# Kernel optimization log

Hardware: AMD Instinct MI355X
Metric: run time of the kernel (lower is better)

Reference implementation:

```python
import jax, jax.numpy as jnp
import numpy as np


def conv1d_same(x, w, b, dilation=1):
    # x: [B, T, Cin], w: [K, Cin, Cout] (WIO), 'same' padding, stride 1
    y = jax.lax.conv_general_dilated(
        x, w, window_strides=(1,), padding='SAME',
        rhs_dilation=(dilation,), dimension_numbers=('NWC', 'WIO', 'NWC'))
    return y + b


def setup_inputs() -> dict:
    key = jax.random.key(0)
    ks = jax.random.split(key, 6)
    B, T, N_IN, N_OUT, ATTN_DIM, KSZ = 16, 2048, 96, 128, 64, 3
    return {
        'x': jax.random.normal(ks[0], (B, T, N_IN), jnp.float32),
        'qkv_w': jax.random.normal(ks[1], (N_IN, 3 * ATTN_DIM), jnp.float32) * 0.05,
        'qkv_b': jnp.zeros((3 * ATTN_DIM,), jnp.float32),
        'scale': jnp.ones((), jnp.float32),
        'conv_w1': jax.random.normal(ks[2], (KSZ, ATTN_DIM, N_OUT), jnp.float32) * 0.05,
        'conv_b1': jnp.zeros((N_OUT,), jnp.float32),
        'conv_w2': jax.random.normal(ks[3], (KSZ, N_OUT, N_OUT), jnp.float32) * 0.05,
        'conv_b2': jnp.zeros((N_OUT,), jnp.float32),
        'down_w': jax.random.normal(ks[4], (N_IN, N_OUT), jnp.float32) * 0.1,
    }


def reference(x, qkv_w, qkv_b, scale, conv_w1, conv_b1, conv_w2, conv_b2, down_w):
    # Dense4Attention: single Dense(3*attn_dim), split into q,k,v
    qkv = x @ qkv_w + qkv_b                       # [B,T,3*D]
    q, k, v = jnp.split(qkv, 3, axis=-1)          # each [B,T,D]
    # AttentionBlock: scores = q k^T * learned scale; non-causal (default)
    scores = jnp.einsum('btd,bsd->bts', q, k) * scale   # [B,T,T]
    weights = jax.nn.softmax(scores, axis=2)            # softmax_axis=2
    out_attn = jnp.einsum('bts,bsd->btd', weights, v)   # [B,T,D]
    h = jax.nn.relu(conv1d_same(out_attn, conv_w1, conv_b1, 1))
    out = jax.nn.relu(conv1d_same(h, conv_w2, conv_b2, 1))   # [B,T,n_out]
    # enhanced residual: softmax over time of row-sums of attn weights
    weight_x = jax.nn.softmax(jnp.sum(weights, axis=2), axis=1)  # [B,T]
    en_res_x = (weight_x[..., None] * x) @ down_w   # n_in != n_out -> downsample
    res = x @ down_w                                 # skip path downsample
    return jax.nn.relu(out + res + en_res_x)
```

## Files before the change

kernel.cpp:

```cpp
#include <hip/hip_runtime.h>
#include <cstdint>

#define B_   16
#define T_   2048
#define CIN  96
#define DH   64
#define NOUT 128

typedef float floatx4 __attribute__((ext_vector_type(4)));
typedef short shortx8 __attribute__((ext_vector_type(8)));
typedef unsigned int uintx2 __attribute__((ext_vector_type(2)));

__device__ __forceinline__ unsigned short f2bf(float f) {
  unsigned int u = __float_as_uint(f);
  u += 0x7FFFu + ((u >> 16) & 1u);
  return (unsigned short)(u >> 16);
}
__device__ __forceinline__ uint32_t cvtpk(float lo, float hi) {
  uint32_t r;
  asm("v_cvt_pk_bf16_f32 %0, %1, %2" : "=v"(r) : "v"(lo), "v"(hi));
  return r;
}
__device__ __forceinline__ floatx4 f4zero() { floatx4 v; v[0]=0.f;v[1]=0.f;v[2]=0.f;v[3]=0.f; return v; }
__device__ __forceinline__ shortx8 s8zero() { shortx8 v;
#pragma unroll
  for (int i=0;i<8;++i) v[i]=0; return v; }

__device__ __forceinline__ void plane_swap(uint32_t& a, uint32_t& b) {
#if __has_builtin(__builtin_amdgcn_permlane32_swap) && __has_builtin(__builtin_amdgcn_permlane16_swap)
  uintx2 r1 = __builtin_amdgcn_permlane32_swap(a, b, false, false);
  uintx2 r2 = __builtin_amdgcn_permlane16_swap(r1[0], r1[1], false, false);
  a = r2[0]; b = r2[1];
#else
  asm volatile("v_permlane32_swap_b32 %0, %1\n\t"
               "v_permlane16_swap_b32 %0, %1"
               : "+v"(a), "+v"(b));
#endif
}

__global__ __launch_bounds__(256) void k_wprep(
    const float* __restrict__ qkv_w, const float* __restrict__ cw1,
    const float* __restrict__ cw2, const float* __restrict__ dw,
    unsigned short* __restrict__ qwt, unsigned short* __restrict__ w1t,
    unsigned short* __restrict__ w2t, unsigned short* __restrict__ dwt)
{
  int o = blockIdx.x * 256 + threadIdx.x;
  if (o < 18432) {
    int co = o / 96, ci = o % 96;
    qwt[o] = f2bf(qkv_w[ci * 192 + co]);
  } else if (o < 43008) {
    int p = o - 18432;
    int tap = p / 8192, rem = p % 8192, co = rem >> 6, ci = rem & 63;
    w1t[p] = f2bf(cw1[(tap * 64 + ci) * 128 + co]);
  } else if (o < 92160) {
    int p = o - 43008;
    int tap = p / 16384, rem = p % 16384, co = rem >> 7, ci = rem & 127;
    w2t[p] = f2bf(cw2[(tap * 128 + ci) * 128 + co]);
  } else if (o < 104448) {
    int p = o - 92160;
    int co = p / 96, ci = p % 96;
    dwt[p] = f2bf(dw[ci * 128 + co]);
  }
}

__global__ __launch_bounds__(256) void k_qkv(
    const float* __restrict__ x, const unsigned short* __restrict__ qwt,
    const float* __restrict__ qkv_b, const float* __restrict__ scale_p,
    unsigned short* __restrict__ qb, unsigned short* __restrict__ kb,
    unsigned short* __restrict__ vT)
{
  __shared__ __align__(16) unsigned short Xs[64][104];
  __shared__ __align__(16) unsigned short Vs[64][72];
  const int bx = blockIdx.x;
  const int b = bx >> 5, t0 = (bx & 31) * 64;
  const int tid = threadIdx.x, wave = tid >> 6, lane = tid & 63;
  const int l15 = lane & 15, quad = lane >> 4;
  const float scl2 = scale_p[0] * 1.4426950408889634f;

  for (int idx = tid; idx < 64 * 24; idx += 256) {
    int r = idx / 24, c = (idx % 24) * 4;
    float4 xv = *(const float4*)(x + ((size_t)(b * T_ + t0 + r)) * CIN + c);
    ushort4 o; o.x = f2bf(xv.x); o.y = f2bf(xv.y); o.z = f2bf(xv.z); o.w = f2bf(xv.w);
    *(ushort4*)(&Xs[r][c]) = o;
  }
  __syncthreads();

  floatx4 acc[4][3];
#pragma unroll
  for (int mt = 0; mt < 4; ++mt)
#pragma unroll
    for (int nt = 0; nt < 3; ++nt) acc[mt][nt] = f4zero();

#pragma unroll
  for (int ks = 0; ks < 3; ++ks) {
    shortx8 wf[3];
#pragma unroll
    for (int nt = 0; nt < 3; ++nt) {
      int j = wave * 48 + nt * 16 + l15;
      wf[nt] = *(const shortx8*)(qwt + (size_t)j * 96 + ks * 32 + quad * 8);
    }
#pragma unroll
    for (int mt = 0; mt < 4; ++mt) {
      shortx8 af = *(const shortx8*)(&Xs[mt * 16 + l15][ks * 32 + quad * 8]);
#pragma unroll
      for (int nt = 0; nt < 3; ++nt)
        acc[mt][nt] = __builtin_amdgcn_mfma_f32_16x16x32_bf16(af, wf[nt], acc[mt][nt], 0, 0, 0);
    }
  }

#pragma unroll
  for (int nt = 0; nt < 3; ++nt) {
    int j0 = wave * 48 + nt * 16;
    int j = j0 + l15;
    float bias = qkv_b[j];
#pragma unroll
    for (int mt = 0; mt < 4; ++mt) {
#pragma unroll
      for (int r = 0; r < 4; ++r) {
        int t = t0 + mt * 16 + quad * 4 + r;
        float v = acc[mt][nt][r] + bias;
        if (j0 < 64)        qb[((size_t)b * T_ + t) * DH + j] = f2bf(v * scl2);
        else if (j0 < 128)  kb[((size_t)b * T_ + t) * DH + (j - 64)] = f2bf(v);
        else                Vs[j - 128][mt * 16 + quad * 4 + r] = f2bf(v);
      }
    }
  }
  __syncthreads();
  for (int idx = tid; idx < 64 * 8; idx += 256) {
    int d = idx >> 3, seg = (idx & 7) * 8;
    *(shortx8*)(vT + ((size_t)b * DH + d) * T_ + t0 + seg) =
        *(const shortx8*)(&Vs[d][seg]);
  }
}

__global__ __launch_bounds__(256) void k_attn(
    const unsigned short* __restrict__ qb, const unsigned short* __restrict__ kb,
    const unsigned short* __restrict__ vT,
    unsigned short* __restrict__ ab)
{
  __shared__ __align__(16) unsigned short Kt[64][72];
  __shared__ __align__(16) unsigned short Vt[80][72];
  const int bx = blockIdx.x;
  const int qt = bx & 31, b = bx >> 5;
  const int tid = threadIdx.x, wave = tid >> 6, lane = tid & 63;
  const int l15 = lane & 15, quad = lane >> 4;

  const unsigned short* qrow = qb + ((size_t)b * T_ + qt * 64 + wave * 16 + l15) * DH;
  shortx8 qf0 = *(const shortx8*)(qrow + quad * 8);
  shortx8 qf1 = *(const shortx8*)(qrow + 32 + quad * 8);

  floatx4 O[5];
#pragma unroll
  for (int i = 0; i < 5; ++i) O[i] = f4zero();

  const unsigned short* kbase = kb + (size_t)b * T_ * DH;
  const unsigned short* vbase = vT + (size_t)b * DH * T_;

  for (int idx = tid; idx < 16 * 72; idx += 256) {
    int r = idx / 72, c = idx % 72;
    Vt[64 + r][c] = (r == 0) ? (unsigned short)0x3F80 : (unsigned short)0;
  }

  const int kr0 = tid >> 3, kc = (tid & 7) * 8;
  shortx8 pk[2], pv[2];
#pragma unroll
  for (int i = 0; i < 2; ++i) {
    pk[i] = *(const shortx8*)(kbase + (size_t)(kr0 + i * 32) * DH + kc);
    pv[i] = *(const shortx8*)(vbase + (size_t)(kr0 + i * 32) * T_ + kc);
  }

  for (int t = 0; t < 32; ++t) {
#pragma unroll
    for (int i = 0; i < 2; ++i) {
      *(shortx8*)(&Kt[kr0 + i * 32][kc]) = pk[i];
      *(shortx8*)(&Vt[kr0 + i * 32][kc]) = pv[i];
    }
    __syncthreads();

    if (t < 31) {
      int s0 = (t + 1) * 64;
#pragma unroll
      for (int i = 0; i < 2; ++i) {
        pk[i] = *(const shortx8*)(kbase + (size_t)(s0 + kr0 + i * 32) * DH + kc);
        pv[i] = *(const shortx8*)(vbase + (size_t)(kr0 + i * 32) * T_ + s0 + kc);
      }
    }

    floatx4 S[4];
#pragma unroll
    for (int nt = 0; nt < 4; ++nt) {
      shortx8 bk0 = *(const shortx8*)(&Kt[nt * 16 + l15][quad * 8]);
      shortx8 bk1 = *(const shortx8*)(&Kt[nt * 16 + l15][32 + quad * 8]);
      S[nt] = f4zero();
      S[nt] = __builtin_amdgcn_mfma_f32_16x16x32_bf16(bk0, qf0, S[nt], 0, 0, 0);
      S[nt] = __builtin_amdgcn_mfma_f32_16x16x32_bf16(bk1, qf1, S[nt], 0, 0, 0);
    }

    uint32_t pkv[8];
#pragma unroll
    for (int nt = 0; nt < 4; ++nt) {
#pragma unroll
      for (int j = 0; j < 2; ++j)
        pkv[nt * 2 + j] = cvtpk(exp2f(S[nt][2 * j]), exp2f(S[nt][2 * j + 1]));
    }

#pragma unroll
    for (int kk = 0; kk < 2; ++kk) {
      uint32_t a0 = pkv[4 * kk + 0], b0 = pkv[4 * kk + 2];
      plane_swap(a0, b0);
      uint32_t a1 = pkv[4 * kk + 1], b1 = pkv[4 * kk + 3];
      plane_swap(a1, b1);
      union { shortx8 s; uint32_t u[4]; } fu;
      fu.u[0] = a0; fu.u[1] = a1; fu.u[2] = b0; fu.u[3] = b1;
#pragma unroll
      for (int dt = 0; dt < 5; ++dt) {
        shortx8 bv = *(const shortx8*)(&Vt[dt * 16 + l15][kk * 32 + quad * 8]);
        O[dt] = __builtin_amdgcn_mfma_f32_16x16x32_bf16(fu.s, bv, O[dt], 0, 0, 0);
      }
    }
    __syncthreads();
  }

  unsigned short* abase = ab + ((size_t)b * T_ + qt * 64 + wave * 16) * DH;
#pragma unroll
  for (int r = 0; r < 4; ++r) {
    float s = __shfl(O[4][r], quad << 4);
    float inv = 1.f / s;
    int row = quad * 4 + r;
#pragma unroll
    for (int dt = 0; dt < 4; ++dt)
      abase[(size_t)row * DH + dt * 16 + l15] = f2bf(O[dt][r] * inv);
  }
}

__global__ __launch_bounds__(256) void k_conv12(
    const unsigned short* __restrict__ ab, const float* __restrict__ x,
    const unsigned short* __restrict__ w1t, const unsigned short* __restrict__ w2t,
    const unsigned short* __restrict__ dwt,
    const float* __restrict__ b1, const float* __restrict__ b2,
    float* __restrict__ out)
{
  __shared__ __align__(16) unsigned short At[82][72];
  __shared__ __align__(16) unsigned short Ht[80][136];
  __shared__ __align__(16) unsigned short Xt[64][104];
  const int bx = blockIdx.x;
  const int b = bx >> 5, t0 = (bx & 31) * 64;
  const int tid = threadIdx.x, wave = tid >> 6, lane = tid & 63;
  const int l15 = lane & 15, quad = lane >> 4;

  for (int idx = tid; idx < 82 * 8; idx += 256) {
    int r = idx >> 3, c = (idx & 7) * 8;
    int t = t0 + r - 9;
    shortx8 v = s8zero();
    if (t >= 0 && t < T_) v = *(const shortx8*)(ab + ((size_t)b * T_ + t) * DH + c);
    *(shortx8*)(&At[r][c]) = v;
  }
  for (int idx = tid; idx < 64 * 24; idx += 256) {
    int r = idx / 24, c = (idx % 24) * 4;
    float4 xv = *(const float4*)(x + ((size_t)(b * T_ + t0 + r)) * CIN + c);
    ushort4 o; o.x = f2bf(xv.x); o.y = f2bf(xv.y); o.z = f2bf(xv.z); o.w = f2bf(xv.w);
    *(ushort4*)(&Xt[r][c]) = o;
  }
  __syncthreads();

  {
    floatx4 acc[5][2];
#pragma unroll
    for (int mt = 0; mt < 5; ++mt) { acc[mt][0] = f4zero(); acc[mt][1] = f4zero(); }

#pragma unroll
    for (int tap = 0; tap < 3; ++tap) {
#pragma unroll
      for (int ks = 0; ks < 2; ++ks) {
        shortx8 wf[2];
#pragma unroll
        for (int ct = 0; ct < 2; ++ct) {
          int co = wave * 32 + ct * 16 + l15;
          wf[ct] = *(const shortx8*)(w1t + ((size_t)tap * 128 + co) * 64 + ks * 32 + quad * 8);
        }
#pragma unroll
        for (int mt = 0; mt < 5; ++mt) {
          shortx8 af = *(const shortx8*)(&At[mt * 16 + l15 + tap][ks * 32 + quad * 8]);
          acc[mt][0] = __builtin_amdgcn_mfma_f32_16x16x32_bf16(af, wf[0], acc[mt][0], 0, 0, 0);
          acc[mt][1] = __builtin_amdgcn_mfma_f32_16x16x32_bf16(af, wf[1], acc[mt][1], 0, 0, 0);
        }
      }
    }

#pragma unroll
    for (int ct = 0; ct < 2; ++ct) {
      int co = wave * 32 + ct * 16 + l15;
      float bias = b1[co];
#pragma unroll
      for (int mt = 0; mt < 5; ++mt)
#pragma unroll
        for (int r = 0; r < 4; ++r) {
          int hr = mt * 16 + quad * 4 + r;
          int t = t0 - 8 + hr;
          unsigned short hv = 0;
          if (t >= 0 && t < T_) hv = f2bf(fmaxf(acc[mt][ct][r] + bias, 0.f));
          Ht[hr][co] = hv;
        }
    }
  }
  __syncthreads();

  floatx4 a2[4][2], ar[4][2];
#pragma unroll
  for (int mt = 0; mt < 4; ++mt) { a2[mt][0]=f4zero(); a2[mt][1]=f4zero(); ar[mt][0]=f4zero(); ar[mt][1]=f4zero(); }

#pragma unroll
  for (int tap = 0; tap < 3; ++tap) {
#pragma unroll
    for (int ks = 0; ks < 4; ++ks) {
      shortx8 wf[2];
#pragma unroll
      for (int ct = 0; ct < 2; ++ct) {
        int co = wave * 32 + ct * 16 + l15;
        wf[ct] = *(const shortx8*)(w2t + ((size_t)tap * 128 + co) * 128 + ks * 32 + quad * 8);
      }
#pragma unroll
      for (int mt = 0; mt < 4; ++mt) {
        shortx8 af = *(const shortx8*)(&Ht[mt * 16 + l15 + 7 + tap][ks * 32 + quad * 8]);
        a2[mt][0] = __builtin_amdgcn_mfma_f32_16x16x32_bf16(af, wf[0], a2[mt][0], 0, 0, 0);
        a2[mt][1] = __builtin_amdgcn_mfma_f32_16x16x32_bf16(af, wf[1], a2[mt][1], 0, 0, 0);
      }
    }
  }
#pragma unroll
  for (int ks = 0; ks < 3; ++ks) {
    shortx8 wf[2];
#pragma unroll
    for (int ct = 0; ct < 2; ++ct) {
      int co = wave * 32 + ct * 16 + l15;
      wf[ct] = *(const shortx8*)(dwt + (size_t)co * 96 + ks * 32 + quad * 8);
    }
#pragma unroll
    for (int mt = 0; mt < 4; ++mt) {
      shortx8 af = *(const shortx8*)(&Xt[mt * 16 + l15][ks * 32 + quad * 8]);
      ar[mt][0] = __builtin_amdgcn_mfma_f32_16x16x32_bf16(af, wf[0], ar[mt][0], 0, 0, 0);
      ar[mt][1] = __builtin_amdgcn_mfma_f32_16x16x32_bf16(af, wf[1], ar[mt][1], 0, 0, 0);
    }
  }

  const float kres = 1.0f + 1.0f / 2048.0f;
#pragma unroll
  for (int ct = 0; ct < 2; ++ct) {
    int co = wave * 32 + ct * 16 + l15;
    float bias = b2[co];
#pragma unroll
    for (int mt = 0; mt < 4; ++mt)
#pragma unroll
      for (int r = 0; r < 4; ++r) {
        int t = t0 + mt * 16 + quad * 4 + r;
        float o2 = fmaxf(a2[mt][ct][r] + bias, 0.f);
        out[((size_t)b * T_ + t) * NOUT + co] = fmaxf(o2 + ar[mt][ct][r] * kres, 0.f);
      }
  }
}

extern "C" void kernel_launch(void* const* d_in, const int* in_sizes, int n_in,
                              void* d_out, int out_size, void* d_ws, size_t ws_size,
                              hipStream_t stream) {
  const float* x      = (const float*)d_in[0];
  const float* qkv_w  = (const float*)d_in[1];
  const float* qkv_b  = (const float*)d_in[2];
  const float* scale  = (const float*)d_in[3];
  const float* cw1    = (const float*)d_in[4];
  const float* cb1    = (const float*)d_in[5];
  const float* cw2    = (const float*)d_in[6];
  const float* cb2    = (const float*)d_in[7];
  const float* dw     = (const float*)d_in[8];

  char* ws = (char*)d_ws;
  unsigned short* qb  = (unsigned short*)(ws + 0);
  unsigned short* kb  = (unsigned short*)(ws + 4194304);
  unsigned short* vT  = (unsigned short*)(ws + 8388608);
  unsigned short* ab  = (unsigned short*)(ws + 12582912);
  unsigned short* qwt = (unsigned short*)(ws + 25165824);
  unsigned short* w1t = (unsigned short*)(ws + 25202688);
  unsigned short* w2t = (unsigned short*)(ws + 25251840);
  unsigned short* dwt = (unsigned short*)(ws + 25350144);

  k_wprep <<<408, 256, 0, stream>>>(qkv_w, cw1, cw2, dw, qwt, w1t, w2t, dwt);
  k_qkv   <<<512, 256, 0, stream>>>(x, qwt, qkv_b, scale, qb, kb, vT);
  k_attn  <<<512, 256, 0, stream>>>(qb, kb, vT, ab);
  k_conv12<<<512, 256, 0, stream>>>(ab, x, w1t, w2t, dwt, cb1, cb2, (float*)d_out);
}
```

Before: 143.2 us.

## Split attention keys across waves with register-direct loads and LDS reduction

The attention kernel now has each wave handle all 64 queries of the block over a disjoint quarter of the key range, loading K and V fragments straight from global memory into registers. This removes the shared-memory K/V staging and the per-tile block barriers. Partial outputs and row sums are combined at the end through a shared-memory reduction. The row sum is now accumulated with VALU adds instead of an extra ones-column MFMA. In exchange the kernel holds more accumulator registers, uses more LDS for the reduction buffers, and does uncoalesced global loads that now go through cache rather than LDS.

```diff
diff --git a/kernel.cpp b/kernel.cpp
--- a/kernel.cpp
+++ b/kernel.cpp
@@ -138,98 +138,114 @@
     const unsigned short* __restrict__ vT,
     unsigned short* __restrict__ ab)
 {
-  __shared__ __align__(16) unsigned short Kt[64][72];
-  __shared__ __align__(16) unsigned short Vt[80][72];
+  __shared__ __align__(16) float OL[4][64][68];
+  __shared__ float SL[4][64];
   const int bx = blockIdx.x;
   const int qt = bx & 31, b = bx >> 5;
   const int tid = threadIdx.x, wave = tid >> 6, lane = tid & 63;
   const int l15 = lane & 15, quad = lane >> 4;
 
-  const unsigned short* qrow = qb + ((size_t)b * T_ + qt * 64 + wave * 16 + l15) * DH;
-  shortx8 qf0 = *(const shortx8*)(qrow + quad * 8);
-  shortx8 qf1 = *(const shortx8*)(qrow + 32 + quad * 8);
-
-  floatx4 O[5];
-#pragma unroll
-  for (int i = 0; i < 5; ++i) O[i] = f4zero();
+  shortx8 qf[4][2];
+#pragma unroll
+  for (int qg = 0; qg < 4; ++qg) {
+    const unsigned short* qrow = qb + ((size_t)b * T_ + qt * 64 + qg * 16 + l15) * DH;
+    qf[qg][0] = *(const shortx8*)(qrow + quad * 8);
+    qf[qg][1] = *(const shortx8*)(qrow + 32 + quad * 8);
+  }
+
+  floatx4 O[4][4];
+#pragma unroll
+  for (int qg = 0; qg < 4; ++qg)
+#pragma unroll
+    for (int dt = 0; dt < 4; ++dt) O[qg][dt] = f4zero();
+  float lsum[4] = {0.f, 0.f, 0.f, 0.f};
 
   const unsigned short* kbase = kb + (size_t)b * T_ * DH;
   const unsigned short* vbase = vT + (size_t)b * DH * T_;
 
-  for (int idx = tid; idx < 16 * 72; idx += 256) {
-    int r = idx / 72, c = idx % 72;
-    Vt[64 + r][c] = (r == 0) ? (unsigned short)0x3F80 : (unsigned short)0;
-  }
-
-  const int kr0 = tid >> 3, kc = (tid & 7) * 8;
-  shortx8 pk[2], pv[2];
-#pragma unroll
-  for (int i = 0; i < 2; ++i) {
-    pk[i] = *(const shortx8*)(kbase + (size_t)(kr0 + i * 32) * DH + kc);
-    pv[i] = *(const shortx8*)(vbase + (size_t)(kr0 + i * 32) * T_ + kc);
-  }
-
-  for (int t = 0; t < 32; ++t) {
-#pragma unroll
-    for (int i = 0; i < 2; ++i) {
-      *(shortx8*)(&Kt[kr0 + i * 32][kc]) = pk[i];
-      *(shortx8*)(&Vt[kr0 + i * 32][kc]) = pv[i];
-    }
-    __syncthreads();
-
-    if (t < 31) {
-      int s0 = (t + 1) * 64;
-#pragma unroll
-      for (int i = 0; i < 2; ++i) {
-        pk[i] = *(const shortx8*)(kbase + (size_t)(s0 + kr0 + i * 32) * DH + kc);
-        pv[i] = *(const shortx8*)(vbase + (size_t)(kr0 + i * 32) * T_ + s0 + kc);
-      }
-    }
-
-    floatx4 S[4];
+  for (int ti = 0; ti < 8; ++ti) {
+    const int s0 = (ti * 4 + wave) * 64;
+    shortx8 bk[4][2], bv[2][4];
 #pragma unroll
     for (int nt = 0; nt < 4; ++nt) {
-      shortx8 bk0 = *(const shortx8*)(&Kt[nt * 16 + l15][quad * 8]);
-      shortx8 bk1 = *(const shortx8*)(&Kt[nt * 16 + l15][32 + quad * 8]);
-      S[nt] = f4zero();
-      S[nt] = __builtin_amdgcn_mfma_f32_16x16x32_bf16(bk0, qf0, S[nt], 0, 0, 0);
-      S[nt] = __builtin_amdgcn_mfma_f32_16x16x32_bf16(bk1, qf1, S[nt], 0, 0, 0);
-    }
-
-    uint32_t pkv[8];
-#pragma unroll
-    for (int nt = 0; nt < 4; ++nt) {
-#pragma unroll
-      for (int j = 0; j < 2; ++j)
-        pkv[nt * 2 + j] = cvtpk(exp2f(S[nt][2 * j]), exp2f(S[nt][2 * j + 1]));
-    }
-
-#pragma unroll
-    for (int kk = 0; kk < 2; ++kk) {
-      uint32_t a0 = pkv[4 * kk + 0], b0 = pkv[4 * kk + 2];
-      plane_swap(a0, b0);
-      uint32_t a1 = pkv[4 * kk + 1], b1 = pkv[4 * kk + 3];
-      plane_swap(a1, b1);
-      union { shortx8 s; uint32_t u[4]; } fu;
-      fu.u[0] = a0; fu.u[1] = a1; fu.u[2] = b0; fu.u[3] = b1;
-#pragma unroll
-      for (int dt = 0; dt < 5; ++dt) {
-        shortx8 bv = *(const shortx8*)(&Vt[dt * 16 + l15][kk * 32 + quad * 8]);
-        O[dt] = __builtin_amdgcn_mfma_f32_16x16x32_bf16(fu.s, bv, O[dt], 0, 0, 0);
-      }
-    }
-    __syncthreads();
-  }
-
-  unsigned short* abase = ab + ((size_t)b * T_ + qt * 64 + wave * 16) * DH;
-#pragma unroll
-  for (int r = 0; r < 4; ++r) {
-    float s = __shfl(O[4][r], quad << 4);
-    float inv = 1.f / s;
-    int row = quad * 4 + r;
+      const unsigned short* kr = kbase + (size_t)(s0 + nt * 16 + l15) * DH;
+      bk[nt][0] = *(const shortx8*)(kr + quad * 8);
+      bk[nt][1] = *(const shortx8*)(kr + 32 + quad * 8);
+    }
+#pragma unroll
+    for (int kk = 0; kk < 2; ++kk)
+#pragma unroll
+      for (int dt = 0; dt < 4; ++dt)
+        bv[kk][dt] = *(const shortx8*)(vbase + (size_t)(dt * 16 + l15) * T_ + s0 + kk * 32 + quad * 8);
+
+#pragma unroll
+    for (int qg = 0; qg < 4; ++qg) {
+      floatx4 S[4];
+#pragma unroll
+      for (int nt = 0; nt < 4; ++nt) {
+        S[nt] = f4zero();
+        S[nt] = __builtin_amdgcn_mfma_f32_16x16x32_bf16(bk[nt][0], qf[qg][0], S[nt], 0, 0, 0);
+        S[nt] = __builtin_amdgcn_mfma_f32_16x16x32_bf16(bk[nt][1], qf[qg][1], S[nt], 0, 0, 0);
+      }
+      uint32_t pkv[8];
+#pragma unroll
+      for (int nt = 0; nt < 4; ++nt)
+#pragma unroll
+        for (int j = 0; j < 2; ++j) {
+          float lo = exp2f(S[nt][2 * j]);
+          float hi = exp2f(S[nt][2 * j + 1]);
+          lsum[qg] += lo + hi;
+          pkv[nt * 2 + j] = cvtpk(lo, hi);
+        }
+#pragma unroll
+      for (int kk = 0; kk < 2; ++kk) {
+        uint32_t a0 = pkv[4 * kk + 0], b0 = pkv[4 * kk + 2];
+        plane_swap(a0, b0);
+        uint32_t a1 = pkv[4 * kk + 1], b1 = pkv[4 * kk + 3];
+        plane_swap(a1, b1);
+        union { shortx8 s; uint32_t u[4]; } fu;
+        fu.u[0] = a0; fu.u[1] = a1; fu.u[2] = b0; fu.u[3] = b1;
+#pragma unroll
+        for (int dt = 0; dt < 4; ++dt)
+          O[qg][dt] = __builtin_amdgcn_mfma_f32_16x16x32_bf16(fu.s, bv[kk][dt], O[qg][dt], 0, 0, 0);
+      }
+    }
+  }
+
+#pragma unroll
+  for (int qg = 0; qg < 4; ++qg) {
+    float v = lsum[qg];
+    v += __shfl_xor(v, 16);
+    v += __shfl_xor(v, 32);
+    if (lane < 16) SL[wave][qg * 16 + lane] = v;
 #pragma unroll
     for (int dt = 0; dt < 4; ++dt)
-      abase[(size_t)row * DH + dt * 16 + l15] = f2bf(O[dt][r] * inv);
+#pragma unroll
+      for (int r = 0; r < 4; ++r)
+        OL[wave][qg * 16 + quad * 4 + r][dt * 16 + l15] = O[qg][dt][r];
+  }
+  __syncthreads();
+
+  {
+    const int q = tid >> 2, d0 = (tid & 3) * 16;
+    float inv = 1.f / (SL[0][q] + SL[1][q] + SL[2][q] + SL[3][q]);
+    unsigned short outv[16];
+#pragma unroll
+    for (int i = 0; i < 16; i += 4) {
+      floatx4 s = *(const floatx4*)&OL[0][q][d0 + i];
+#pragma unroll
+      for (int w = 1; w < 4; ++w) {
+        floatx4 t = *(const floatx4*)&OL[w][q][d0 + i];
+        s[0] += t[0]; s[1] += t[1]; s[2] += t[2]; s[3] += t[3];
+      }
+      outv[i]     = f2bf(s[0] * inv);
+      outv[i + 1] = f2bf(s[1] * inv);
+      outv[i + 2] = f2bf(s[2] * inv);
+      outv[i + 3] = f2bf(s[3] * inv);
+    }
+    unsigned short* ap = ab + ((size_t)b * T_ + qt * 64 + q) * DH + d0;
+    *(shortx8*)(ap)     = *(const shortx8*)&outv[0];
+    *(shortx8*)(ap + 8) = *(const shortx8*)&outv[8];
   }
 }
 
```

Result: no change. 144.9 us (+1.2%).
